# Kernel optimization log

Measured on AMD Instinct MI355X. Metric: run time of the kernel, lower is better.

The kernel has to match this reference:

```python
import jax, jax.numpy as jnp
import numpy as np

B, S, H, NH, FF, L, BLK, R = 2, 4096, 768, 12, 3072, 4, 64, 3
NB = S // BLK          # 64 blocks
D = H // NH            # 64 per-head dim
A = 3 + 2 + R          # window(3) + global(2) + random(R) attended blocks
EPS = 1e-12
SCALE = 1.0 / np.sqrt(D).astype(np.float32)


def setup_inputs() -> dict:
    key = jax.random.key(0)
    ks = jax.random.split(key, 12)
    p = lambda k, shp: jax.random.normal(k, shp, jnp.float32) * 0.02
    return {
        "input_ids": jax.random.normal(ks[0], (B, S, 4), jnp.float32),
        "rand_blocks": jax.random.randint(ks[1], (NB, R), 0, NB, jnp.int32),
        "emb_w": p(ks[2], (4, H)), "emb_b": jnp.zeros((H,), jnp.float32),
        "ln1_g": jnp.ones((L, H), jnp.float32), "ln1_b": jnp.zeros((L, H), jnp.float32),
        "wq": p(ks[3], (L, H, H)), "bq": jnp.zeros((L, H), jnp.float32),
        "wk": p(ks[4], (L, H, H)), "bk": jnp.zeros((L, H), jnp.float32),
        "wv": p(ks[5], (L, H, H)), "bv": jnp.zeros((L, H), jnp.float32),
        "wo": p(ks[6], (L, H, H)), "bo": jnp.zeros((L, H), jnp.float32),
        "ln2_g": jnp.ones((L, H), jnp.float32), "ln2_b": jnp.zeros((L, H), jnp.float32),
        "w1": p(ks[7], (L, H, FF)), "b1": jnp.zeros((L, FF), jnp.float32),
        "w2": p(ks[8], (L, FF, H)), "b2": jnp.zeros((L, H), jnp.float32),
        "clf_w": p(ks[9], (H, 4)), "clf_b": jnp.zeros((4,), jnp.float32),
    }


def _ln(x, g, b):
    m = x.mean(-1, keepdims=True)
    v = jnp.var(x, axis=-1, keepdims=True)  # biased var, like torch LayerNorm
    return (x - m) * jax.lax.rsqrt(v + EPS) * g + b


def _attend_idx(rand_blocks):
    # per query block: [i-1, i, i+1] window (edge-clamped), global {0, NB-1}, R random
    ar = jnp.arange(NB)
    win = jnp.stack([jnp.clip(ar - 1, 0, NB - 1), ar, jnp.clip(ar + 1, 0, NB - 1)], 1)
    glb = jnp.broadcast_to(jnp.array([0, NB - 1], jnp.int32), (NB, 2))
    return jnp.concatenate([win.astype(jnp.int32), glb, rand_blocks], 1)  # [NB, A]


def _attn(x, wq, bq, wk, bk, wv, bv, wo, bo, idx):
    def heads(t):  # [B,S,H] -> [B,NH,NB,BLK,D]
        return t.reshape(B, NB, BLK, NH, D).transpose(0, 3, 1, 2, 4)
    q = heads(x @ wq + bq)
    k = heads(x @ wk + bk)
    v = heads(x @ wv + bv)
    kg = k[:, :, idx].reshape(B, NH, NB, A * BLK, D)  # gather attended key blocks
    vg = v[:, :, idx].reshape(B, NH, NB, A * BLK, D)
    s = jnp.einsum('bhnqd,bhnkd->bhnqk', q, kg) * SCALE  # [B,NH,NB,BLK,A*BLK]
    p = jax.nn.softmax(s, axis=-1)
    o = jnp.einsum('bhnqk,bhnkd->bhnqd', p, vg)
    o = o.transpose(0, 2, 3, 1, 4).reshape(B, S, H)
    return o @ wo + bo


def reference(input_ids, rand_blocks, emb_w, emb_b, ln1_g, ln1_b, wq, bq, wk, bk,
              wv, bv, wo, bo, ln2_g, ln2_b, w1, b1, w2, b2, clf_w, clf_b):
    idx = _attend_idx(rand_blocks)
    x = input_ids @ emb_w + emb_b
    for l in range(L):
        h = _ln(x, ln1_g[l], ln1_b[l])
        x = x + _attn(h, wq[l], bq[l], wk[l], bk[l], wv[l], bv[l], wo[l], bo[l], idx)
        h = _ln(x, ln2_g[l], ln2_b[l])
        x = x + (jax.nn.gelu(h @ w1[l] + b1[l], approximate=False) @ w2[l] + b2[l])
    logits = x @ clf_w + clf_b
    return jax.nn.softmax(logits, axis=-1)
```

## Files before the change

### kernel.cpp

```cpp
#include <hip/hip_runtime.h>
#include <math.h>

constexpr int B  = 2;
constexpr int S  = 4096;
constexpr int H  = 768;
constexpr int NH = 12;
constexpr int FF = 3072;
constexpr int L  = 4;
constexpr int R  = 3;
constexpr int NB = 64;
constexpr int AB = 8;
constexpr float SCALE = 0.125f;
constexpr int QKV_N = 3 * H;

constexpr int ROWS = B * S;
constexpr size_t XSZ = (size_t)B * S * H;

typedef short bf16x8 __attribute__((ext_vector_type(8)));
typedef unsigned short u16x8 __attribute__((ext_vector_type(8)));
typedef unsigned short u16x4 __attribute__((ext_vector_type(4)));
typedef float f32x4 __attribute__((ext_vector_type(4)));
typedef unsigned short ushort_t;

__device__ __forceinline__ ushort_t f2b(float f) {
  union { float f; unsigned u; } c; c.f = f;
  unsigned r = c.u + 0x7fffu + ((c.u >> 16) & 1u);
  return (ushort_t)(r >> 16);
}

__device__ __forceinline__ float gelu_f(float x) {
  float y = 0.7978845608f * x * (1.0f + 0.044715f * x * x);
  float e = __expf(2.0f * y);
  float th = 1.0f - 2.0f / (e + 1.0f);
  return 0.5f * x * (1.0f + th);
}

__device__ __forceinline__ void gload16(const void* g, void* l) {
  __builtin_amdgcn_global_load_lds(
      (const __attribute__((address_space(1))) unsigned int*)g,
      (__attribute__((address_space(3))) unsigned int*)l, 16, 0, 0);
}

template <int N>
__device__ __forceinline__ void waitvm() {
  if constexpr (N == 0)      { asm volatile("s_waitcnt vmcnt(0)" ::: "memory"); }
  else if constexpr (N == 4) { asm volatile("s_waitcnt vmcnt(4)" ::: "memory"); }
  else                       { asm volatile("s_waitcnt vmcnt(6)" ::: "memory"); }
}

__global__ __launch_bounds__(256) void embed_kernel(
    const float* __restrict__ ids, const float* __restrict__ w,
    const float* __restrict__ bvec, float* __restrict__ x) {
  int i = blockIdx.x * 256 + threadIdx.x;
  if (i >= (int)XSZ) return;
  int hc = i % H;
  int bs = i / H;
  float s = bvec[hc];
  #pragma unroll
  for (int j = 0; j < 4; ++j) s += ids[bs * 4 + j] * w[j * H + hc];
  x[i] = s;
}

__global__ __launch_bounds__(256) void ln_kernel(
    const float* __restrict__ x, const float* __restrict__ g,
    const float* __restrict__ bvec, ushort_t* __restrict__ out) {
  int row = blockIdx.x;
  const float* xr = x + (size_t)row * H;
  int t = threadIdx.x;
  float v0 = xr[t], v1 = xr[t + 256], v2 = xr[t + 512];
  float s  = v0 + v1 + v2;
  float ss = v0 * v0 + v1 * v1 + v2 * v2;
  for (int off = 1; off < 64; off <<= 1) {
    s  += __shfl_xor(s,  off);
    ss += __shfl_xor(ss, off);
  }
  __shared__ float sm[8];
  int w = t >> 6, lane = t & 63;
  if (lane == 0) { sm[w] = s; sm[4 + w] = ss; }
  __syncthreads();
  s  = sm[0] + sm[1] + sm[2] + sm[3];
  ss = sm[4] + sm[5] + sm[6] + sm[7];
  float mean = s * (1.0f / H);
  float var  = ss * (1.0f / H) - mean * mean;
  float rstd = rsqrtf(var + 1e-12f);
  ushort_t* orow = out + (size_t)row * H;
  orow[t]       = f2b((v0 - mean) * rstd * g[t]       + bvec[t]);
  orow[t + 256] = f2b((v1 - mean) * rstd * g[t + 256] + bvec[t + 256]);
  orow[t + 512] = f2b((v2 - mean) * rstd * g[t + 512] + bvec[t + 512]);
}

__global__ __launch_bounds__(256) void tcvt_kernel(
    const float* __restrict__ in, ushort_t* __restrict__ out,
    int K, int N, size_t inZ, size_t outZ) {
  __shared__ float tile[32][33];
  const float* inz = in + blockIdx.z * inZ;
  ushort_t* outz = out + blockIdx.z * outZ;
  int k0 = blockIdx.y * 32, n0 = blockIdx.x * 32;
  int tx = threadIdx.x & 31, ty = threadIdx.x >> 5;
  #pragma unroll
  for (int i = 0; i < 4; ++i) {
    int kk = ty + i * 8;
    tile[kk][tx] = inz[(size_t)(k0 + kk) * N + n0 + tx];
  }
  __syncthreads();
  #pragma unroll
  for (int i = 0; i < 4; ++i) {
    int nn = ty + i * 8;
    outz[(size_t)(n0 + nn) * K + k0 + tx] = f2b(tile[tx][nn]);
  }
}

__global__ __launch_bounds__(256) void concat_bias_kernel(
    const float* __restrict__ bq, const float* __restrict__ bk,
    const float* __restrict__ bv, float* __restrict__ out) {
  int i = blockIdx.x * 256 + threadIdx.x;
  if (i >= L * QKV_N) return;
  int l = i / QKV_N, c = i % QKV_N;
  float val = (c < H) ? bq[l * H + c] : (c < 2 * H) ? bk[l * H + c - H] : bv[l * H + c - 2 * H];
  out[i] = val;
}

template <int BN, int EPI>
__global__ __launch_bounds__(256, (BN == 256 ? 2 : 3)) void bgemm(
    const ushort_t* __restrict__ A, const ushort_t* __restrict__ Wt,
    const float* __restrict__ bias, const float* __restrict__ res,
    float* __restrict__ Cf, ushort_t* __restrict__ Cb, ushort_t* __restrict__ Cv,
    int M, int N, int K, int ncol) {
  constexpr int LDSB = (128 + BN) * 32;
  constexpr int NLD  = (128 + BN) / 64;
  constexpr int NI   = BN / 32;
  __shared__ ushort_t lds[3 * LDSB];

  const int nwg = (int)gridDim.x;
  const int qq = nwg >> 3, r0 = nwg & 7;
  const int xcd = (int)blockIdx.x & 7, loc = (int)blockIdx.x >> 3;
  const int swz = (xcd < r0 ? xcd * (qq + 1) : r0 * (qq + 1) + (xcd - r0) * qq) + loc;
  const int bm = (swz / ncol) * 128, bn = (swz % ncol) * BN;

  const int t = threadIdx.x;
  const int wid = t >> 6, lane = t & 63;
  const int fcol = lane & 15, fgrp = lane >> 4;
  const int wm = wid >> 1, wn = wid & 1;

  const ushort_t* src[NLD];
  int dst[NLD];
  #pragma unroll
  for (int j = 0; j < NLD; ++j) {
    int idx = j * 2048 + t * 8;
    dst[j] = idx;
    int ch = (idx >> 3) & 3;
    int row;
    const ushort_t* base;
    if (idx < 4096) { row = idx >> 5;           base = A  + (size_t)(bm + row) * K; }
    else            { row = (idx - 4096) >> 5;  base = Wt + (size_t)(bn + row) * K; }
    src[j] = base + ((ch ^ ((row >> 1) & 3)) << 3);
  }

  int aoff[4], boff[NI];
  #pragma unroll
  for (int mi = 0; mi < 4; ++mi) {
    int row = wm * 64 + mi * 16 + fcol;
    aoff[mi] = row * 32 + ((fgrp ^ ((row >> 1) & 3)) << 3);
  }
  #pragma unroll
  for (int ni = 0; ni < NI; ++ni) {
    int row = wn * (BN / 2) + ni * 16 + fcol;
    boff[ni] = 4096 + row * 32 + ((fgrp ^ ((row >> 1) & 3)) << 3);
  }

  f32x4 acc[4][NI] = {};

  #pragma unroll
  for (int j = 0; j < NLD; ++j) gload16(src[j], &lds[dst[j]]);
  #pragma unroll
  for (int j = 0; j < NLD; ++j) gload16(src[j] + 32, &lds[LDSB + dst[j]]);
  int kgl = 64;

#define GEMM_STEP(P, DOSTAGE, WN)                                          \
  {                                                                        \
    waitvm<WN>();                                                          \
    __builtin_amdgcn_sched_barrier(0);                                     \
    __builtin_amdgcn_s_barrier();                                          \
    __builtin_amdgcn_sched_barrier(0);                                     \
    if (DOSTAGE) {                                                         \
      _Pragma("unroll")                                                    \
      for (int j = 0; j < NLD; ++j)                                        \
        gload16(src[j] + kgl, &lds[(((P) + 2) % 3) * LDSB + dst[j]]);      \
      kgl += 32;                                                           \
    }                                                                      \
    bf16x8 af[4], bfr[NI];                                                 \
    _Pragma("unroll")                                                      \
    for (int mi = 0; mi < 4; ++mi)                                         \
      af[mi] = *(const bf16x8*)&lds[(P) * LDSB + aoff[mi]];                \
    _Pragma("unroll")                                                      \
    for (int ni = 0; ni < NI; ++ni)                                        \
      bfr[ni] = *(const bf16x8*)&lds[(P) * LDSB + boff[ni]];               \
    __builtin_amdgcn_s_setprio(1);                                         \
    _Pragma("unroll")                                                      \
    for (int mi = 0; mi < 4; ++mi)                                         \
      _Pragma("unroll")                                                    \
      for (int ni = 0; ni < NI; ++ni)                                      \
        acc[mi][ni] = __builtin_amdgcn_mfma_f32_16x16x32_bf16(             \
            af[mi], bfr[ni], acc[mi][ni], 0, 0, 0);                        \
    __builtin_amdgcn_s_setprio(0);                                         \
  }

  const int NT = K >> 5;
  for (int tau = 0; tau < NT - 3; tau += 3) {
    GEMM_STEP(0, true, NLD)
    GEMM_STEP(1, true, NLD)
    GEMM_STEP(2, true, NLD)
  }
  GEMM_STEP(0, true,  NLD)
  GEMM_STEP(1, false, NLD)
  GEMM_STEP(2, false, 0)
#undef GEMM_STEP

  if (EPI == 0 && bn >= 2 * H) {
    #pragma unroll
    for (int mi = 0; mi < 4; ++mi) {
      const int m = bm + wm * 64 + mi * 16 + fgrp * 4;
      #pragma unroll
      for (int ni = 0; ni < NI; ++ni) {
        const int n = bn + wn * (BN / 2) + ni * 16 + fcol;
        const float bb = bias[n];
        u16x4 pk;
        #pragma unroll
        for (int r = 0; r < 4; ++r) pk[r] = f2b(acc[mi][ni][r] + bb);
        *(u16x4*)&Cv[(size_t)(n - 2 * H) * M + m] = pk;
      }
    }
    return;
  }
  #pragma unroll
  for (int mi = 0; mi < 4; ++mi) {
    const int m = bm + wm * 64 + mi * 16 + fgrp * 4;
    #pragma unroll
    for (int ni = 0; ni < NI; ++ni) {
      const int n = bn + wn * (BN / 2) + ni * 16 + fcol;
      const float bb = bias[n];
      #pragma unroll
      for (int r = 0; r < 4; ++r) {
        float val = acc[mi][ni][r] + bb;
        if (EPI == 1) {
          Cf[(size_t)(m + r) * N + n] = val + res[(size_t)(m + r) * N + n];
        } else if (EPI == 2) {
          Cb[(size_t)(m + r) * N + n] = f2b(gelu_f(val));
        } else {
          Cb[(size_t)(m + r) * N + n] = f2b(val);
        }
      }
    }
  }
}

__global__ __launch_bounds__(256) void attn_mfma(
    const ushort_t* __restrict__ qkv, const ushort_t* __restrict__ vT,
    const int* __restrict__ rb, ushort_t* __restrict__ ao) {
  __shared__ ushort_t Ks[2][64 * 72];
  __shared__ ushort_t Vt[2][64 * 72];
  __shared__ ushort_t Ps[4][16 * 72];
  const int n = blockIdx.x, hh = blockIdx.y, b = blockIdx.z;
  const int t = threadIdx.x;
  const int wid = t >> 6, lane = t & 63;
  const int fcol = lane & 15, fgrp = lane >> 4;
  const int qr0 = n * 64 + wid * 16;

  bf16x8 qf[2];
  #pragma unroll
  for (int kc = 0; kc < 2; ++kc)
    qf[kc] = *(const bf16x8*)&qkv[((size_t)(b * S) + qr0 + fcol) * QKV_N + hh * 64 + kc * 32 + fgrp * 8];

  f32x4 oacc[4] = {};
  float mrow[4], lrow[4];
  #pragma unroll
  for (int r = 0; r < 4; ++r) { mrow[r] = -1e30f; lrow[r] = 0.f; }

  int kbs[AB];
  kbs[0] = (n > 0) ? n - 1 : 0;
  kbs[1] = n;
  kbs[2] = (n < NB - 1) ? n + 1 : NB - 1;
  kbs[3] = 0;
  kbs[4] = NB - 1;
  kbs[5] = rb[n * R + 0];
  kbs[6] = rb[n * R + 1];
  kbs[7] = rb[n * R + 2];

  const ushort_t* kbase = qkv + (size_t)(b * S) * QKV_N + H + hh * 64;
  const ushort_t* vbase = vT + (size_t)(hh * 64) * ROWS + b * S;

  const int srow = t >> 3;
  const int soff = (t & 7) * 8;

  {
    const int kb = kbs[0];
    u16x8 k0 = *(const u16x8*)&kbase[(size_t)(kb * 64 + srow) * QKV_N + soff];
    u16x8 k1 = *(const u16x8*)&kbase[(size_t)(kb * 64 + srow + 32) * QKV_N + soff];
    u16x8 v0 = *(const u16x8*)&vbase[(size_t)srow * ROWS + kb * 64 + soff];
    u16x8 v1 = *(const u16x8*)&vbase[(size_t)(srow + 32) * ROWS + kb * 64 + soff];
    *(u16x8*)&Ks[0][srow * 72 + soff]        = k0;
    *(u16x8*)&Ks[0][(srow + 32) * 72 + soff] = k1;
    *(u16x8*)&Vt[0][srow * 72 + soff]        = v0;
    *(u16x8*)&Vt[0][(srow + 32) * 72 + soff] = v1;
  }
  __syncthreads();

  for (int a = 0; a < AB; ++a) {
    const int buf = a & 1;

    u16x8 pk0, pk1, pv0, pv1;
    if (a + 1 < AB) {
      const int kb = kbs[a + 1];
      pk0 = *(const u16x8*)&kbase[(size_t)(kb * 64 + srow) * QKV_N + soff];
      pk1 = *(const u16x8*)&kbase[(size_t)(kb * 64 + srow + 32) * QKV_N + soff];
      pv0 = *(const u16x8*)&vbase[(size_t)srow * ROWS + kb * 64 + soff];
      pv1 = *(const u16x8*)&vbase[(size_t)(srow + 32) * ROWS + kb * 64 + soff];
    }

    f32x4 sacc[4] = {};
    __builtin_amdgcn_s_setprio(1);
    #pragma unroll
    for (int ni = 0; ni < 4; ++ni)
      #pragma unroll
      for (int kc = 0; kc < 2; ++kc) {
        bf16x8 kf = *(const bf16x8*)&Ks[buf][(ni * 16 + fcol) * 72 + kc * 32 + fgrp * 8];
        sacc[ni] = __builtin_amdgcn_mfma_f32_16x16x32_bf16(qf[kc], kf, sacc[ni], 0, 0, 0);
      }
    __builtin_amdgcn_s_setprio(0);

    #pragma unroll
    for (int ni = 0; ni < 4; ++ni)
      #pragma unroll
      for (int r = 0; r < 4; ++r) sacc[ni][r] *= SCALE;
    #pragma unroll
    for (int r = 0; r < 4; ++r) {
      float tm = fmaxf(fmaxf(sacc[0][r], sacc[1][r]), fmaxf(sacc[2][r], sacc[3][r]));
      tm = fmaxf(tm, __shfl_xor(tm, 1));
      tm = fmaxf(tm, __shfl_xor(tm, 2));
      tm = fmaxf(tm, __shfl_xor(tm, 4));
      tm = fmaxf(tm, __shfl_xor(tm, 8));
      float mn = fmaxf(mrow[r], tm);
      float corr = __expf(mrow[r] - mn);
      mrow[r] = mn;
      float rs = 0.f;
      #pragma unroll
      for (int ni = 0; ni < 4; ++ni) {
        float p = __expf(sacc[ni][r] - mn);
        sacc[ni][r] = p;
        rs += p;
      }
      rs += __shfl_xor(rs, 1);
      rs += __shfl_xor(rs, 2);
      rs += __shfl_xor(rs, 4);
      rs += __shfl_xor(rs, 8);
      lrow[r] = lrow[r] * corr + rs;
      #pragma unroll
      for (int ni = 0; ni < 4; ++ni) oacc[ni][r] *= corr;
    }

    if (a + 1 < AB) {
      *(u16x8*)&Ks[buf ^ 1][srow * 72 + soff]        = pk0;
      *(u16x8*)&Ks[buf ^ 1][(srow + 32) * 72 + soff] = pk1;
      *(u16x8*)&Vt[buf ^ 1][srow * 72 + soff]        = pv0;
      *(u16x8*)&Vt[buf ^ 1][(srow + 32) * 72 + soff] = pv1;
    }

    #pragma unroll
    for (int ni = 0; ni < 4; ++ni)
      #pragma unroll
      for (int r = 0; r < 4; ++r)
        Ps[wid][(fgrp * 4 + r) * 72 + ni * 16 + fcol] = f2b(sacc[ni][r]);

    bf16x8 pa[2];
    #pragma unroll
    for (int kc = 0; kc < 2; ++kc)
      pa[kc] = *(const bf16x8*)&Ps[wid][fcol * 72 + kc * 32 + fgrp * 8];

    __builtin_amdgcn_s_setprio(1);
    #pragma unroll
    for (int kc = 0; kc < 2; ++kc)
      #pragma unroll
      for (int ni = 0; ni < 4; ++ni) {
        bf16x8 vb = *(const bf16x8*)&Vt[buf][(ni * 16 + fcol) * 72 + kc * 32 + fgrp * 8];
        oacc[ni] = __builtin_amdgcn_mfma_f32_16x16x32_bf16(pa[kc], vb, oacc[ni], 0, 0, 0);
      }
    __builtin_amdgcn_s_setprio(0);

    __syncthreads();
  }

  #pragma unroll
  for (int r = 0; r < 4; ++r) {
    float inv = 1.0f / lrow[r];
    int row = qr0 + fgrp * 4 + r;
    #pragma unroll
    for (int ni = 0; ni < 4; ++ni)
      ao[((size_t)(b * S) + row) * H + hh * 64 + ni * 16 + fcol] = f2b(oacc[ni][r] * inv);
  }
}

__global__ __launch_bounds__(64) void clf_kernel(
    const float* __restrict__ x, const float* __restrict__ w,
    const float* __restrict__ bvec, float* __restrict__ out) {
  int row = blockIdx.x;
  int lane = threadIdx.x;
  const float* xr = x + (size_t)row * H;
  float p0 = 0.f, p1 = 0.f, p2 = 0.f, p3 = 0.f;
  for (int d = lane; d < H; d += 64) {
    float xv = xr[d];
    p0 += xv * w[d * 4 + 0];
    p1 += xv * w[d * 4 + 1];
    p2 += xv * w[d * 4 + 2];
    p3 += xv * w[d * 4 + 3];
  }
  for (int off = 1; off < 64; off <<= 1) {
    p0 += __shfl_xor(p0, off);
    p1 += __shfl_xor(p1, off);
    p2 += __shfl_xor(p2, off);
    p3 += __shfl_xor(p3, off);
  }
  if (lane == 0) {
    float l0 = p0 + bvec[0], l1 = p1 + bvec[1], l2 = p2 + bvec[2], l3 = p3 + bvec[3];
    float mx = fmaxf(fmaxf(l0, l1), fmaxf(l2, l3));
    float e0 = __expf(l0 - mx), e1 = __expf(l1 - mx), e2 = __expf(l2 - mx), e3 = __expf(l3 - mx);
    float inv = 1.0f / (e0 + e1 + e2 + e3);
    out[row * 4 + 0] = e0 * inv;
    out[row * 4 + 1] = e1 * inv;
    out[row * 4 + 2] = e2 * inv;
    out[row * 4 + 3] = e3 * inv;
  }
}

extern "C" void kernel_launch(void* const* d_in, const int* in_sizes, int n_in,
                              void* d_out, int out_size, void* d_ws, size_t ws_size,
                              hipStream_t stream) {
  const float* input_ids = (const float*)d_in[0];
  const int*   rand_bl   = (const int*)  d_in[1];
  const float* emb_w = (const float*)d_in[2];
  const float* emb_b = (const float*)d_in[3];
  const float* ln1_g = (const float*)d_in[4];
  const float* ln1_b = (const float*)d_in[5];
  const float* wq = (const float*)d_in[6];
  const float* bq = (const float*)d_in[7];
  const float* wk = (const float*)d_in[8];
  const float* bk = (const float*)d_in[9];
  const float* wv = (const float*)d_in[10];
  const float* bv = (const float*)d_in[11];
  const float* wo = (const float*)d_in[12];
  const float* bo = (const float*)d_in[13];
  const float* ln2_g = (const float*)d_in[14];
  const float* ln2_b = (const float*)d_in[15];
  const float* w1 = (const float*)d_in[16];
  const float* b1 = (const float*)d_in[17];
  const float* w2 = (const float*)d_in[18];
  const float* b2 = (const float*)d_in[19];
  const float* clf_w = (const float*)d_in[20];
  const float* clf_b = (const float*)d_in[21];

  char* p = (char*)d_ws;
  float*    x    = (float*)p;    p += XSZ * 4;
  ushort_t* h    = (ushort_t*)p; p += XSZ * 2;
  ushort_t* qkv  = (ushort_t*)p; p += (size_t)ROWS * QKV_N * 2;
  ushort_t* ao   = (ushort_t*)p; p += XSZ * 2;
  ushort_t* ff   = qkv;
  ushort_t* vT   = (ushort_t*)p; p += (size_t)H * ROWS * 2;
  ushort_t* qkvT = (ushort_t*)p; p += (size_t)L * QKV_N * H * 2;
  ushort_t* woT  = (ushort_t*)p; p += (size_t)L * H * H * 2;
  ushort_t* w1T  = (ushort_t*)p; p += (size_t)L * H * FF * 2;
  ushort_t* w2T  = (ushort_t*)p; p += (size_t)L * FF * H * 2;
  float*    bqkv = (float*)p;    p += (size_t)L * QKV_N * 4;

  tcvt_kernel<<<dim3(H / 32, H / 32, L), 256, 0, stream>>>(
      wq, qkvT + 0 * H * H, H, H, (size_t)H * H, (size_t)QKV_N * H);
  tcvt_kernel<<<dim3(H / 32, H / 32, L), 256, 0, stream>>>(
      wk, qkvT + 1 * H * H, H, H, (size_t)H * H, (size_t)QKV_N * H);
  tcvt_kernel<<<dim3(H / 32, H / 32, L), 256, 0, stream>>>(
      wv, qkvT + 2 * H * H, H, H, (size_t)H * H, (size_t)QKV_N * H);
  tcvt_kernel<<<dim3(H / 32, H / 32, L), 256, 0, stream>>>(
      wo, woT, H, H, (size_t)H * H, (size_t)H * H);
  tcvt_kernel<<<dim3(FF / 32, H / 32, L), 256, 0, stream>>>(
      w1, w1T, H, FF, (size_t)H * FF, (size_t)H * FF);
  tcvt_kernel<<<dim3(H / 32, FF / 32, L), 256, 0, stream>>>(
      w2, w2T, FF, H, (size_t)FF * H, (size_t)FF * H);
  concat_bias_kernel<<<(L * QKV_N + 255) / 256, 256, 0, stream>>>(bq, bk, bv, bqkv);

  embed_kernel<<<(int)((XSZ + 255) / 256), 256, 0, stream>>>(input_ids, emb_w, emb_b, x);

  for (int l = 0; l < L; ++l) {
    ln_kernel<<<ROWS, 256, 0, stream>>>(x, ln1_g + l * H, ln1_b + l * H, h);

    bgemm<256, 0><<<(ROWS / 128) * (QKV_N / 256), 256, 0, stream>>>(
        h, qkvT + (size_t)l * QKV_N * H, bqkv + l * QKV_N, nullptr,
        nullptr, qkv, vT, ROWS, QKV_N, H, QKV_N / 256);

    attn_mfma<<<dim3(NB, NH, B), 256, 0, stream>>>(qkv, vT, rand_bl, ao);

    bgemm<128, 1><<<(ROWS / 128) * (H / 128), 256, 0, stream>>>(
        ao, woT + (size_t)l * H * H, bo + l * H, x, x, nullptr, nullptr, ROWS, H, H, H / 128);

    ln_kernel<<<ROWS, 256, 0, stream>>>(x, ln2_g + l * H, ln2_b + l * H, h);

    bgemm<256, 2><<<(ROWS / 128) * (FF / 256), 256, 0, stream>>>(
        h, w1T + (size_t)l * H * FF, b1 + l * FF, nullptr,
        nullptr, ff, nullptr, ROWS, FF, H, FF / 256);

    bgemm<128, 1><<<(ROWS / 128) * (H / 128), 256, 0, stream>>>(
        ff, w2T + (size_t)l * FF * H, b2 + l * H, x, x, nullptr, nullptr, ROWS, H, FF, H / 128);
  }

  clf_kernel<<<ROWS, 64, 0, stream>>>(x, clf_w, clf_b, (float*)d_out);
}
```

Before: 1.004 ms.

## Use 256x256-tile 8-wave GEMM with phased LDS double buffering for QKV and FFN1

Adds a new GEMM kernel with 512 threads (8 waves) computing 256x256 output tiles, used for the QKV projection and the FFN up-projection. Each K-step of 64 is double-buffered in a 64K-element LDS buffer and split into four phases that interleave global-to-LDS staging with MFMA work on half of the M fragments. B fragments are reused across both halves. The larger tile raises arithmetic intensity and cuts redundant global loads, at the cost of more LDS and registers per workgroup and fewer workgroups in the grid. The older GEMM is reduced to a 128x128 residual-add variant.

```diff
diff --git a/kernel.cpp b/kernel.cpp
--- a/kernel.cpp
+++ b/kernel.cpp
@@ -120,22 +120,170 @@
   out[i] = val;
 }
 
-template <int BN, int EPI>
-__global__ __launch_bounds__(256, (BN == 256 ? 2 : 3)) void bgemm(
+template <int EPI>
+__global__ __launch_bounds__(512, 2) void bgemm8p(
     const ushort_t* __restrict__ A, const ushort_t* __restrict__ Wt,
-    const float* __restrict__ bias, const float* __restrict__ res,
-    float* __restrict__ Cf, ushort_t* __restrict__ Cb, ushort_t* __restrict__ Cv,
+    const float* __restrict__ bias,
+    ushort_t* __restrict__ Cb, ushort_t* __restrict__ Cv,
     int M, int N, int K, int ncol) {
-  constexpr int LDSB = (128 + BN) * 32;
-  constexpr int NLD  = (128 + BN) / 64;
-  constexpr int NI   = BN / 32;
-  __shared__ ushort_t lds[3 * LDSB];
+  __shared__ ushort_t lds[65536];
 
   const int nwg = (int)gridDim.x;
   const int qq = nwg >> 3, r0 = nwg & 7;
   const int xcd = (int)blockIdx.x & 7, loc = (int)blockIdx.x >> 3;
   const int swz = (xcd < r0 ? xcd * (qq + 1) : r0 * (qq + 1) + (xcd - r0) * qq) + loc;
-  const int bm = (swz / ncol) * 128, bn = (swz % ncol) * BN;
+  const int bm = (swz / ncol) * 256, bn = (swz % ncol) * 256;
+
+  const int t = threadIdx.x;
+  const int wid = t >> 6, lane = t & 63;
+  const int fcol = lane & 15, fgrp = lane >> 4;
+  const int wm = wid >> 2, wn = wid & 3;
+
+  const ushort_t* srcA[2];
+  const ushort_t* srcB[2];
+  int cdst[2];
+  #pragma unroll
+  for (int j = 0; j < 2; ++j) {
+    int idx = j * 4096 + t * 8;
+    cdst[j] = idx;
+    int row = idx >> 5;
+    int ch  = (idx >> 3) & 3;
+    int so  = (ch ^ ((row >> 1) & 3)) << 3;
+    srcA[j] = A  + (size_t)(bm + row) * K + so;
+    srcB[j] = Wt + (size_t)(bn + row) * K + so;
+  }
+
+  int aoff[8], boff[4];
+  #pragma unroll
+  for (int mi = 0; mi < 8; ++mi) {
+    int row = wm * 128 + mi * 16 + fcol;
+    aoff[mi] = row * 32 + ((fgrp ^ ((row >> 1) & 3)) << 3);
+  }
+  #pragma unroll
+  for (int ni = 0; ni < 4; ++ni) {
+    int row = wn * 64 + ni * 16 + fcol;
+    boff[ni] = 16384 + row * 32 + ((fgrp ^ ((row >> 1) & 3)) << 3);
+  }
+
+  f32x4 acc[8][4] = {};
+  bf16x8 bfr[4];
+
+  #pragma unroll
+  for (int j = 0; j < 2; ++j) gload16(srcA[j],      &lds[0     + cdst[j]]);
+  #pragma unroll
+  for (int j = 0; j < 2; ++j) gload16(srcB[j],      &lds[16384 + cdst[j]]);
+  #pragma unroll
+  for (int j = 0; j < 2; ++j) gload16(srcA[j] + 32, &lds[8192  + cdst[j]]);
+  #pragma unroll
+  for (int j = 0; j < 2; ++j) gload16(srcB[j] + 32, &lds[24576 + cdst[j]]);
+  int kgl = 64;
+
+#define PHASE8(BUF, Q, DOST, WN)                                             \
+  {                                                                          \
+    if ((Q) == 0 || (Q) == 2) {                                              \
+      waitvm<WN>();                                                          \
+      __builtin_amdgcn_sched_barrier(0);                                     \
+    }                                                                        \
+    __builtin_amdgcn_s_barrier();                                            \
+    __builtin_amdgcn_sched_barrier(0);                                       \
+    if (DOST) {                                                              \
+      const int sc_kc  = ((Q) >= 2) ? 1 : 0;                                 \
+      const int sc_isB = ((Q) & 1);                                          \
+      const int sc_dst = (1 - (BUF)) * 32768 + sc_isB * 16384 + sc_kc * 8192;\
+      _Pragma("unroll")                                                      \
+      for (int j = 0; j < 2; ++j)                                            \
+        gload16((sc_isB ? srcB[j] : srcA[j]) + kgl + sc_kc * 32,             \
+                &lds[sc_dst + cdst[j]]);                                     \
+    }                                                                        \
+    {                                                                        \
+      const int kc_ = (Q) >> 1, h_ = (Q) & 1;                                \
+      bf16x8 af[4];                                                          \
+      _Pragma("unroll")                                                      \
+      for (int i = 0; i < 4; ++i)                                            \
+        af[i] = *(const bf16x8*)&lds[(BUF) * 32768 + kc_ * 8192 + aoff[h_ * 4 + i]]; \
+      if (h_ == 0) {                                                         \
+        _Pragma("unroll")                                                    \
+        for (int ni = 0; ni < 4; ++ni)                                       \
+          bfr[ni] = *(const bf16x8*)&lds[(BUF) * 32768 + kc_ * 8192 + boff[ni]]; \
+      }                                                                      \
+      __builtin_amdgcn_s_setprio(1);                                         \
+      _Pragma("unroll")                                                      \
+      for (int i = 0; i < 4; ++i)                                            \
+        _Pragma("unroll")                                                    \
+        for (int ni = 0; ni < 4; ++ni)                                       \
+          acc[h_ * 4 + i][ni] = __builtin_amdgcn_mfma_f32_16x16x32_bf16(     \
+              af[i], bfr[ni], acc[h_ * 4 + i][ni], 0, 0, 0);                 \
+      __builtin_amdgcn_s_setprio(0);                                         \
+    }                                                                        \
+  }
+
+#define TILE8(BUF, DOST, LWN)   \
+  PHASE8(BUF, 0, DOST, 4)       \
+  PHASE8(BUF, 1, DOST, 4)       \
+  PHASE8(BUF, 2, DOST, LWN)     \
+  PHASE8(BUF, 3, DOST, 4)       \
+  kgl += 64;
+
+  const int NT = K >> 6;
+  for (int tt = 0; tt < NT - 2; tt += 2) {
+    TILE8(0, true, 4)
+    TILE8(1, true, 4)
+  }
+  TILE8(0, true, 4)
+  PHASE8(1, 0, false, 4)
+  PHASE8(1, 1, false, 4)
+  PHASE8(1, 2, false, 0)
+  PHASE8(1, 3, false, 4)
+#undef TILE8
+#undef PHASE8
+
+  if (EPI == 0 && bn >= 2 * H) {
+    #pragma unroll
+    for (int mi = 0; mi < 8; ++mi) {
+      const int m = bm + wm * 128 + mi * 16 + fgrp * 4;
+      #pragma unroll
+      for (int ni = 0; ni < 4; ++ni) {
+        const int n = bn + wn * 64 + ni * 16 + fcol;
+        const float bb = bias[n];
+        u16x4 pk;
+        #pragma unroll
+        for (int r = 0; r < 4; ++r) pk[r] = f2b(acc[mi][ni][r] + bb);
+        *(u16x4*)&Cv[(size_t)(n - 2 * H) * M + m] = pk;
+      }
+    }
+    return;
+  }
+  #pragma unroll
+  for (int mi = 0; mi < 8; ++mi) {
+    const int m = bm + wm * 128 + mi * 16 + fgrp * 4;
+    #pragma unroll
+    for (int ni = 0; ni < 4; ++ni) {
+      const int n = bn + wn * 64 + ni * 16 + fcol;
+      const float bb = bias[n];
+      #pragma unroll
+      for (int r = 0; r < 4; ++r) {
+        float val = acc[mi][ni][r] + bb;
+        if (EPI == 2) val = gelu_f(val);
+        Cb[(size_t)(m + r) * N + n] = f2b(val);
+      }
+    }
+  }
+}
+
+template <int EPI>
+__global__ __launch_bounds__(256, 3) void bgemm(
+    const ushort_t* __restrict__ A, const ushort_t* __restrict__ Wt,
+    const float* __restrict__ bias, const float* __restrict__ res,
+    float* __restrict__ Cf, int M, int N, int K, int ncol) {
+  constexpr int LDSB = 8192;
+  constexpr int NLD  = 4;
+  __shared__ ushort_t lds[3 * LDSB];
+
+  const int nwg = (int)gridDim.x;
+  const int qq = nwg >> 3, r0 = nwg & 7;
+  const int xcd = (int)blockIdx.x & 7, loc = (int)blockIdx.x >> 3;
+  const int swz = (xcd < r0 ? xcd * (qq + 1) : r0 * (qq + 1) + (xcd - r0) * qq) + loc;
+  const int bm = (swz / ncol) * 128, bn = (swz % ncol) * 128;
 
   const int t = threadIdx.x;
   const int wid = t >> 6, lane = t & 63;
@@ -156,19 +304,19 @@
     src[j] = base + ((ch ^ ((row >> 1) & 3)) << 3);
   }
 
-  int aoff[4], boff[NI];
+  int aoff[4], boff[4];
   #pragma unroll
   for (int mi = 0; mi < 4; ++mi) {
     int row = wm * 64 + mi * 16 + fcol;
     aoff[mi] = row * 32 + ((fgrp ^ ((row >> 1) & 3)) << 3);
   }
   #pragma unroll
-  for (int ni = 0; ni < NI; ++ni) {
-    int row = wn * (BN / 2) + ni * 16 + fcol;
+  for (int ni = 0; ni < 4; ++ni) {
+    int row = wn * 64 + ni * 16 + fcol;
     boff[ni] = 4096 + row * 32 + ((fgrp ^ ((row >> 1) & 3)) << 3);
   }
 
-  f32x4 acc[4][NI] = {};
+  f32x4 acc[4][4] = {};
 
   #pragma unroll
   for (int j = 0; j < NLD; ++j) gload16(src[j], &lds[dst[j]]);
@@ -188,18 +336,18 @@
         gload16(src[j] + kgl, &lds[(((P) + 2) % 3) * LDSB + dst[j]]);      \
       kgl += 32;                                                           \
     }                                                                      \
-    bf16x8 af[4], bfr[NI];                                                 \
+    bf16x8 af[4], bfr[4];                                                  \
     _Pragma("unroll")                                                      \
     for (int mi = 0; mi < 4; ++mi)                                         \
       af[mi] = *(const bf16x8*)&lds[(P) * LDSB + aoff[mi]];                \
     _Pragma("unroll")                                                      \
-    for (int ni = 0; ni < NI; ++ni)                                        \
+    for (int ni = 0; ni < 4; ++ni)                                         \
       bfr[ni] = *(const bf16x8*)&lds[(P) * LDSB + boff[ni]];               \
     __builtin_amdgcn_s_setprio(1);                                         \
     _Pragma("unroll")                                                      \
     for (int mi = 0; mi < 4; ++mi)                                         \
       _Pragma("unroll")                                                    \
-      for (int ni = 0; ni < NI; ++ni)                                      \
+      for (int ni = 0; ni < 4; ++ni)                                       \
         acc[mi][ni] = __builtin_amdgcn_mfma_f32_16x16x32_bf16(             \
             af[mi], bfr[ni], acc[mi][ni], 0, 0, 0);                        \
     __builtin_amdgcn_s_setprio(0);                                         \
@@ -207,48 +355,26 @@
 
   const int NT = K >> 5;
   for (int tau = 0; tau < NT - 3; tau += 3) {
-    GEMM_STEP(0, true, NLD)
-    GEMM_STEP(1, true, NLD)
-    GEMM_STEP(2, true, NLD)
-  }
-  GEMM_STEP(0, true,  NLD)
-  GEMM_STEP(1, false, NLD)
+    GEMM_STEP(0, true, 4)
+    GEMM_STEP(1, true, 4)
+    GEMM_STEP(2, true, 4)
+  }
+  GEMM_STEP(0, true,  4)
+  GEMM_STEP(1, false, 4)
   GEMM_STEP(2, false, 0)
 #undef GEMM_STEP
 
-  if (EPI == 0 && bn >= 2 * H) {
-    #pragma unroll
-    for (int mi = 0; mi < 4; ++mi) {
-      const int m = bm + wm * 64 + mi * 16 + fgrp * 4;
-      #pragma unroll
-      for (int ni = 0; ni < NI; ++ni) {
-        const int n = bn + wn * (BN / 2) + ni * 16 + fcol;
-        const float bb = bias[n];
-        u16x4 pk;
-        #pragma unroll
-        for (int r = 0; r < 4; ++r) pk[r] = f2b(acc[mi][ni][r] + bb);
-        *(u16x4*)&Cv[(size_t)(n - 2 * H) * M + m] = pk;
-      }
-    }
-    return;
-  }
   #pragma unroll
   for (int mi = 0; mi < 4; ++mi) {
     const int m = bm + wm * 64 + mi * 16 + fgrp * 4;
     #pragma unroll
-    for (int ni = 0; ni < NI; ++ni) {
-      const int n = bn + wn * (BN / 2) + ni * 16 + fcol;
+    for (int ni = 0; ni < 4; ++ni) {
+      const int n = bn + wn * 64 + ni * 16 + fcol;
       const float bb = bias[n];
       #pragma unroll
       for (int r = 0; r < 4; ++r) {
         float val = acc[mi][ni][r] + bb;
-        if (EPI == 1) {
-          Cf[(size_t)(m + r) * N + n] = val + res[(size_t)(m + r) * N + n];
-        } else if (EPI == 2) {
-          Cb[(size_t)(m + r) * N + n] = f2b(gelu_f(val));
-        } else {
-          Cb[(size_t)(m + r) * N + n] = f2b(val);
-        }
+        Cf[(size_t)(m + r) * N + n] = val + res[(size_t)(m + r) * N + n];
       }
     }
   }
@@ -489,23 +615,23 @@
   for (int l = 0; l < L; ++l) {
     ln_kernel<<<ROWS, 256, 0, stream>>>(x, ln1_g + l * H, ln1_b + l * H, h);
 
-    bgemm<256, 0><<<(ROWS / 128) * (QKV_N / 256), 256, 0, stream>>>(
-        h, qkvT + (size_t)l * QKV_N * H, bqkv + l * QKV_N, nullptr,
-        nullptr, qkv, vT, ROWS, QKV_N, H, QKV_N / 256);
+    bgemm8p<0><<<(ROWS / 256) * (QKV_N / 256), 512, 0, stream>>>(
+        h, qkvT + (size_t)l * QKV_N * H, bqkv + l * QKV_N,
+        qkv, vT, ROWS, QKV_N, H, QKV_N / 256);
 
     attn_mfma<<<dim3(NB, NH, B), 256, 0, stream>>>(qkv, vT, rand_bl, ao);
 
-    bgemm<128, 1><<<(ROWS / 128) * (H / 128), 256, 0, stream>>>(
-        ao, woT + (size_t)l * H * H, bo + l * H, x, x, nullptr, nullptr, ROWS, H, H, H / 128);
+    bgemm<1><<<(ROWS / 128) * (H / 128), 256, 0, stream>>>(
+        ao, woT + (size_t)l * H * H, bo + l * H, x, x, ROWS, H, H, H / 128);
 
     ln_kernel<<<ROWS, 256, 0, stream>>>(x, ln2_g + l * H, ln2_b + l * H, h);
 
-    bgemm<256, 2><<<(ROWS / 128) * (FF / 256), 256, 0, stream>>>(
-        h, w1T + (size_t)l * H * FF, b1 + l * FF, nullptr,
-        nullptr, ff, nullptr, ROWS, FF, H, FF / 256);
-
-    bgemm<128, 1><<<(ROWS / 128) * (H / 128), 256, 0, stream>>>(
-        ff, w2T + (size_t)l * FF * H, b2 + l * H, x, x, nullptr, nullptr, ROWS, H, FF, H / 128);
+    bgemm8p<2><<<(ROWS / 256) * (FF / 256), 512, 0, stream>>>(
+        h, w1T + (size_t)l * H * FF, b1 + l * FF,
+        ff, nullptr, ROWS, FF, H, FF / 256);
+
+    bgemm<1><<<(ROWS / 128) * (H / 128), 256, 0, stream>>>(
+        ff, w2T + (size_t)l * FF * H, b2 + l * H, x, x, ROWS, H, FF, H / 128);
   }
 
   clf_kernel<<<ROWS, 64, 0, stream>>>(x, clf_w, clf_b, (float*)d_out);
```

Measured after the change: 1.069 ms. 6.5% more time.

## Store residual stream in bf16 and use DPP row reductions in attention softmax

Applied to the files above, without the earlier changes.

The residual activation x moves from fp32 to bf16 storage, so the embed, layernorm, classifier and residual-add GEMM epilogues read and write half the bytes. The attention softmax replaces its shuffle-xor max/sum reductions across 16 lanes with DPP row operations. The GEMM step's wait count is fixed at 4 instead of NLD. Rounding the residual to bf16 at every layer builds up precision loss across layers, and the fixed wait count is only correct when NLD matches 4.

```diff
diff --git a/kernel.cpp b/kernel.cpp
--- a/kernel.cpp
+++ b/kernel.cpp
@@ -27,6 +27,10 @@
   unsigned r = c.u + 0x7fffu + ((c.u >> 16) & 1u);
   return (ushort_t)(r >> 16);
 }
+__device__ __forceinline__ float b2f(ushort_t u) {
+  union { float f; unsigned u; } c; c.u = ((unsigned)u) << 16;
+  return c.f;
+}
 
 __device__ __forceinline__ float gelu_f(float x) {
   float y = 0.7978845608f * x * (1.0f + 0.044715f * x * x);
@@ -48,9 +52,30 @@
   else                       { asm volatile("s_waitcnt vmcnt(6)" ::: "memory"); }
 }
 
+template <int CTRL>
+__device__ __forceinline__ float dppmv(float x) {
+  union { float f; int i; } c; c.f = x;
+  c.i = __builtin_amdgcn_update_dpp(c.i, c.i, CTRL, 0xF, 0xF, true);
+  return c.f;
+}
+__device__ __forceinline__ float redmax16(float x) {
+  x = fmaxf(x, dppmv<0xB1>(x));
+  x = fmaxf(x, dppmv<0x4E>(x));
+  x = fmaxf(x, dppmv<0x124>(x));
+  x = fmaxf(x, dppmv<0x128>(x));
+  return x;
+}
+__device__ __forceinline__ float redsum16(float x) {
+  x += dppmv<0xB1>(x);
+  x += dppmv<0x4E>(x);
+  x += dppmv<0x124>(x);
+  x += dppmv<0x128>(x);
+  return x;
+}
+
 __global__ __launch_bounds__(256) void embed_kernel(
     const float* __restrict__ ids, const float* __restrict__ w,
-    const float* __restrict__ bvec, float* __restrict__ x) {
+    const float* __restrict__ bvec, ushort_t* __restrict__ x) {
   int i = blockIdx.x * 256 + threadIdx.x;
   if (i >= (int)XSZ) return;
   int hc = i % H;
@@ -58,16 +83,16 @@
   float s = bvec[hc];
   #pragma unroll
   for (int j = 0; j < 4; ++j) s += ids[bs * 4 + j] * w[j * H + hc];
-  x[i] = s;
+  x[i] = f2b(s);
 }
 
 __global__ __launch_bounds__(256) void ln_kernel(
-    const float* __restrict__ x, const float* __restrict__ g,
+    const ushort_t* __restrict__ x, const float* __restrict__ g,
     const float* __restrict__ bvec, ushort_t* __restrict__ out) {
   int row = blockIdx.x;
-  const float* xr = x + (size_t)row * H;
+  const ushort_t* xr = x + (size_t)row * H;
   int t = threadIdx.x;
-  float v0 = xr[t], v1 = xr[t + 256], v2 = xr[t + 512];
+  float v0 = b2f(xr[t]), v1 = b2f(xr[t + 256]), v2 = b2f(xr[t + 512]);
   float s  = v0 + v1 + v2;
   float ss = v0 * v0 + v1 * v1 + v2 * v2;
   for (int off = 1; off < 64; off <<= 1) {
@@ -123,8 +148,8 @@
 template <int BN, int EPI>
 __global__ __launch_bounds__(256, (BN == 256 ? 2 : 3)) void bgemm(
     const ushort_t* __restrict__ A, const ushort_t* __restrict__ Wt,
-    const float* __restrict__ bias, const float* __restrict__ res,
-    float* __restrict__ Cf, ushort_t* __restrict__ Cb, ushort_t* __restrict__ Cv,
+    const float* __restrict__ bias, const ushort_t* __restrict__ res,
+    ushort_t* __restrict__ Cb, ushort_t* __restrict__ Cv,
     int M, int N, int K, int ncol) {
   constexpr int LDSB = (128 + BN) * 32;
   constexpr int NLD  = (128 + BN) / 64;
@@ -207,12 +232,12 @@
 
   const int NT = K >> 5;
   for (int tau = 0; tau < NT - 3; tau += 3) {
-    GEMM_STEP(0, true, NLD)
-    GEMM_STEP(1, true, NLD)
-    GEMM_STEP(2, true, NLD)
-  }
-  GEMM_STEP(0, true,  NLD)
-  GEMM_STEP(1, false, NLD)
+    GEMM_STEP(0, true, 4)
+    GEMM_STEP(1, true, 4)
+    GEMM_STEP(2, true, 4)
+  }
+  GEMM_STEP(0, true,  4)
+  GEMM_STEP(1, false, 4)
   GEMM_STEP(2, false, 0)
 #undef GEMM_STEP
 
@@ -243,7 +268,8 @@
       for (int r = 0; r < 4; ++r) {
         float val = acc[mi][ni][r] + bb;
         if (EPI == 1) {
-          Cf[(size_t)(m + r) * N + n] = val + res[(size_t)(m + r) * N + n];
+          val += b2f(res[(size_t)(m + r) * N + n]);
+          Cb[(size_t)(m + r) * N + n] = f2b(val);
         } else if (EPI == 2) {
           Cb[(size_t)(m + r) * N + n] = f2b(gelu_f(val));
         } else {
@@ -335,10 +361,7 @@
     #pragma unroll
     for (int r = 0; r < 4; ++r) {
       float tm = fmaxf(fmaxf(sacc[0][r], sacc[1][r]), fmaxf(sacc[2][r], sacc[3][r]));
-      tm = fmaxf(tm, __shfl_xor(tm, 1));
-      tm = fmaxf(tm, __shfl_xor(tm, 2));
-      tm = fmaxf(tm, __shfl_xor(tm, 4));
-      tm = fmaxf(tm, __shfl_xor(tm, 8));
+      tm = redmax16(tm);
       float mn = fmaxf(mrow[r], tm);
       float corr = __expf(mrow[r] - mn);
       mrow[r] = mn;
@@ -349,10 +372,7 @@
         sacc[ni][r] = p;
         rs += p;
       }
-      rs += __shfl_xor(rs, 1);
-      rs += __shfl_xor(rs, 2);
-      rs += __shfl_xor(rs, 4);
-      rs += __shfl_xor(rs, 8);
+      rs = redsum16(rs);
       lrow[r] = lrow[r] * corr + rs;
       #pragma unroll
       for (int ni = 0; ni < 4; ++ni) oacc[ni][r] *= corr;
@@ -400,14 +420,14 @@
 }
 
 __global__ __launch_bounds__(64) void clf_kernel(
-    const float* __restrict__ x, const float* __restrict__ w,
+    const ushort_t* __restrict__ x, const float* __restrict__ w,
     const float* __restrict__ bvec, float* __restrict__ out) {
   int row = blockIdx.x;
   int lane = threadIdx.x;
-  const float* xr = x + (size_t)row * H;
+  const ushort_t* xr = x + (size_t)row * H;
   float p0 = 0.f, p1 = 0.f, p2 = 0.f, p3 = 0.f;
   for (int d = lane; d < H; d += 64) {
-    float xv = xr[d];
+    float xv = b2f(xr[d]);
     p0 += xv * w[d * 4 + 0];
     p1 += xv * w[d * 4 + 1];
     p2 += xv * w[d * 4 + 2];
@@ -458,7 +478,7 @@
   const float* clf_b = (const float*)d_in[21];
 
   char* p = (char*)d_ws;
-  float*    x    = (float*)p;    p += XSZ * 4;
+  ushort_t* x    = (ushort_t*)p; p += XSZ * 2;
   ushort_t* h    = (ushort_t*)p; p += XSZ * 2;
   ushort_t* qkv  = (ushort_t*)p; p += (size_t)ROWS * QKV_N * 2;
   ushort_t* ao   = (ushort_t*)p; p += XSZ * 2;
@@ -491,21 +511,21 @@
 
     bgemm<256, 0><<<(ROWS / 128) * (QKV_N / 256), 256, 0, stream>>>(
         h, qkvT + (size_t)l * QKV_N * H, bqkv + l * QKV_N, nullptr,
-        nullptr, qkv, vT, ROWS, QKV_N, H, QKV_N / 256);
+        qkv, vT, ROWS, QKV_N, H, QKV_N / 256);
 
     attn_mfma<<<dim3(NB, NH, B), 256, 0, stream>>>(qkv, vT, rand_bl, ao);
 
     bgemm<128, 1><<<(ROWS / 128) * (H / 128), 256, 0, stream>>>(
-        ao, woT + (size_t)l * H * H, bo + l * H, x, x, nullptr, nullptr, ROWS, H, H, H / 128);
+        ao, woT + (size_t)l * H * H, bo + l * H, x, x, nullptr, ROWS, H, H, H / 128);
 
     ln_kernel<<<ROWS, 256, 0, stream>>>(x, ln2_g + l * H, ln2_b + l * H, h);
 
     bgemm<256, 2><<<(ROWS / 128) * (FF / 256), 256, 0, stream>>>(
         h, w1T + (size_t)l * H * FF, b1 + l * FF, nullptr,
-        nullptr, ff, nullptr, ROWS, FF, H, FF / 256);
+        ff, nullptr, ROWS, FF, H, FF / 256);
 
     bgemm<128, 1><<<(ROWS / 128) * (H / 128), 256, 0, stream>>>(
-        ff, w2T + (size_t)l * FF * H, b2 + l * H, x, x, nullptr, nullptr, ROWS, H, FF, H / 128);
+        ff, w2T + (size_t)l * FF * H, b2 + l * H, x, x, nullptr, ROWS, H, FF, H / 128);
   }
 
   clf_kernel<<<ROWS, 64, 0, stream>>>(x, clf_w, clf_b, (float*)d_out);
```

Measured after the change: 957.2 us. -4.7%, faster.
